# Kernel tuning notes

Measured on AMD Instinct MI355X. Metric: run time of the kernel, lower is better.

The kernel has to match this reference:

```python
import jax, jax.numpy as jnp
from jax import lax
import numpy as np

C_IN, H, W = 9, 11, 11
N_FILT = 64
N_LAYERS = 8
FC_UNITS = 64
LSTM_H = 64
N_ACTIONS = 6
B, T = 32, 128


def setup_inputs() -> dict:
    key = jax.random.key(0)
    ks = jax.random.split(key, 24)
    s = 0.05
    d = {}
    d['x'] = jax.random.normal(ks[0], (B, T, C_IN, H, W), dtype=jnp.float32)
    d['conv0_w'] = jax.random.normal(ks[1], (N_FILT, C_IN, 3, 3), dtype=jnp.float32) * s
    d['conv0_b'] = jnp.zeros((N_FILT,), jnp.float32)
    d['conv_ws'] = jax.random.normal(ks[2], (N_LAYERS - 1, N_FILT, N_FILT, 3, 3), dtype=jnp.float32) * s
    d['conv_bs'] = jnp.zeros((N_LAYERS - 1, N_FILT), jnp.float32)
    d['fc_w'] = jax.random.normal(ks[3], (FC_UNITS, N_FILT * H * W), dtype=jnp.float32) * s
    d['fc_b'] = jnp.zeros((FC_UNITS,), jnp.float32)
    d['w_ih'] = jax.random.normal(ks[4], (4 * LSTM_H, FC_UNITS), dtype=jnp.float32) * s
    d['w_hh'] = jax.random.normal(ks[5], (4 * LSTM_H, LSTM_H), dtype=jnp.float32) * s
    d['b_ih'] = jnp.zeros((4 * LSTM_H,), jnp.float32)
    d['b_hh'] = jnp.zeros((4 * LSTM_H,), jnp.float32)
    d['p1_w'] = jax.random.normal(ks[6], (128, LSTM_H), dtype=jnp.float32) * s
    d['p1_b'] = jnp.zeros((128,), jnp.float32)
    d['p2_w'] = jax.random.normal(ks[7], (N_ACTIONS, 128), dtype=jnp.float32) * s
    d['p2_b'] = jnp.zeros((N_ACTIONS,), jnp.float32)
    d['v1_w'] = jax.random.normal(ks[8], (128, LSTM_H), dtype=jnp.float32) * s
    d['v1_b'] = jnp.zeros((128,), jnp.float32)
    d['v2_w'] = jax.random.normal(ks[9], (1, 128), dtype=jnp.float32) * s
    d['v2_b'] = jnp.zeros((1,), jnp.float32)
    return d


def _conv_relu(h, w, b):
    # h: [N, C, H, W], w: [O, I, 3, 3] -> SAME padding, stride 1
    y = lax.conv_general_dilated(h, w, (1, 1), [(1, 1), (1, 1)],
                                 dimension_numbers=('NCHW', 'OIHW', 'NCHW'))
    return jax.nn.relu(y + b[None, :, None, None])


def _forward(x, conv0_w, conv0_b, conv_ws, conv_bs, fc_w, fc_b,
             w_ih, w_hh, b_ih, b_hh, p1_w, p1_b, p2_w, p2_b, v1_w, v1_b, v2_w, v2_b):
    b, t = x.shape[0], x.shape[1]
    h = x.reshape(b * t, C_IN, H, W)          # batch CNN over all frames at once
    h = _conv_relu(h, conv0_w, conv0_b)
    for i in range(N_LAYERS - 1):             # fixed small layer loop
        h = _conv_relu(h, conv_ws[i], conv_bs[i])
    h = h.reshape(b * t, N_FILT * H * W)
    feats = jax.nn.relu(h @ fc_w.T + fc_b)    # [B*T, FC_UNITS]
    feats = feats.reshape(b, t, FC_UNITS)

    # LSTM (PyTorch gate order i, f, g, o)
    def step(carry, xt):
        hprev, cprev = carry
        g = xt @ w_ih.T + hprev @ w_hh.T + b_ih + b_hh
        i_g, f_g, g_g, o_g = jnp.split(g, 4, axis=-1)
        c = jax.nn.sigmoid(f_g) * cprev + jax.nn.sigmoid(i_g) * jnp.tanh(g_g)
        hn = jax.nn.sigmoid(o_g) * jnp.tanh(c)
        return (hn, c), hn

    h0 = jnp.zeros((b, LSTM_H), feats.dtype)
    c0 = jnp.zeros((b, LSTM_H), feats.dtype)
    _, outs = lax.scan(step, (h0, c0), jnp.swapaxes(feats, 0, 1))  # [T, B, H]
    lstm_out = jnp.swapaxes(outs, 0, 1)       # [B, T, H]

    p = jax.nn.relu(lstm_out @ p1_w.T + p1_b) @ p2_w.T + p2_b  # [B, T, n_actions]
    v = jax.nn.relu(lstm_out @ v1_w.T + v1_b) @ v2_w.T + v2_b  # [B, T, 1]
    return p, v


def reference(x, conv0_w, conv0_b, conv_ws, conv_bs, fc_w, fc_b,
              w_ih, w_hh, b_ih, b_hh, p1_w, p1_b, p2_w, p2_b, v1_w, v1_b, v2_w, v2_b):
    return _forward(x, conv0_w, conv0_b, conv_ws, conv_bs, fc_w, fc_b,
                    w_ih, w_hh, b_ih, b_hh, p1_w, p1_b, p2_w, p2_b,
                    v1_w, v1_b, v2_w, v2_b)
```

## Files before the change

kernel.cpp:

```cpp
#include <hip/hip_runtime.h>
#include <hip/hip_bf16.h>

typedef __attribute__((ext_vector_type(8))) short short8;
typedef __attribute__((ext_vector_type(4))) short short4_t;
typedef __attribute__((ext_vector_type(4))) float floatx4;
typedef __attribute__((ext_vector_type(16))) float floatx16;

#define MFMA_B16(a,b,c) __builtin_amdgcn_mfma_f32_16x16x32_bf16((a),(b),(c),0,0,0)
#define MFMA32(a,b,c)   __builtin_amdgcn_mfma_f32_32x32x16_bf16((a),(b),(c),0,0,0)

__device__ __forceinline__ short f2bf(float f) {
    union { __hip_bfloat16 h; short s; } u;
    u.h = __float2bfloat16(f);
    return u.s;
}

union S8U { short4_t h[2]; short8 v; };

#define N_FRAMES 4096
#define C_IN     9
#define POS      121
#define NF       64
#define FC_K     7744
#define ISTR     20
#define FSZ      10816

#define OFF_W0    0
#define OFF_WP    18432
#define OFF_FCP   534528
#define OFF_WIHT  1525760
#define OFF_BSUM  1591296
#define OFF_ACTS  1592320
#define OFF_XG    66079744
#define OFF_HOUT  70274048

__global__ __launch_bounds__(256) void prep_kernel(
    const float* __restrict__ conv0_w, const float* __restrict__ conv_ws,
    const float* __restrict__ w_ih,
    const float* __restrict__ b_ih, const float* __restrict__ b_hh,
    const float* __restrict__ fc_w,
    short* __restrict__ w0, short* __restrict__ wpk,
    float* __restrict__ wihT, float* __restrict__ bsum,
    short* __restrict__ fcp)
{
    __shared__ float row[FC_K];
    const int tid = threadIdx.x;
    if (blockIdx.x < 64) {
        const int u = blockIdx.x;
        const float* src = fc_w + (size_t)u*FC_K;
        for (int i = tid; i < FC_K; i += 256) row[i] = src[i];
        __syncthreads();
        short* dst = fcp + (size_t)u*FC_K;
        for (int k2 = tid; k2 < FC_K; k2 += 256) {
            int p = k2 >> 6, c = k2 & 63;
            dst[k2] = f2bf(row[c*121 + p]);
        }
        return;
    }
    int idx = (blockIdx.x - 64)*256 + tid;
    if (idx < 9216) {
        int tap = idx >> 10; int r = idx & 1023;
        int mt = r >> 9; int o = (r >> 4) & 31; int ci = r & 15;
        int oc = mt*32 + o;
        float v = (ci < 9) ? conv0_w[(oc*9 + ci)*9 + tap] : 0.f;
        w0[idx] = f2bf(v);
        return;
    }
    idx -= 9216;
    if (idx < 258048) {
        int l = idx / 36864; int r = idx % 36864;
        int tap = r >> 12; int rr = r & 4095;
        int mt = rr >> 11;
        int ks = (rr >> 9) & 3;
        int o  = (rr >> 4) & 31;
        int ci16 = rr & 15;
        int oc = mt*32 + o;
        int ci = ks*16 + ci16;
        wpk[idx] = f2bf(conv_ws[((l*64 + oc)*64 + ci)*9 + tap]);
        return;
    }
    idx -= 258048;
    if (idx < 16384) {
        int k = idx >> 8; int g = idx & 255;
        wihT[idx] = w_ih[g*64 + k];
        return;
    }
    idx -= 16384;
    if (idx < 256) bsum[idx] = b_ih[idx] + b_hh[idx];
}

__global__ __launch_bounds__(128, 3) void conv_stack(
    const float* __restrict__ x,
    const float* __restrict__ conv0_b,
    const float* __restrict__ conv_bs,
    const short* __restrict__ w0,
    const short* __restrict__ wpk,
    short* __restrict__ acts_out)
{
    __shared__ alignas(16) short act[FSZ];
    const int tid  = threadIdx.x;
    const int lane = tid & 63;
    const int wv   = tid >> 6;
    const int n    = lane & 31;
    const int kh   = lane >> 5;
    char* actb = (char*)act;

    const short8 zero8 = {0,0,0,0,0,0,0,0};
    const floatx16 fz16 = {};

    for (int i = tid*8; i < 3392; i += 1024) *(short8*)(&act[i]) = zero8;
    __syncthreads();

    {
        const float* xf = x + (size_t)blockIdx.x*(C_IN*POS);
        for (int i = tid; i < C_IN*POS; i += 128) {
            int ci = i / POS;
            int p  = i - ci*POS;
            int yy = p / 11;
            int xx = p - yy*11;
            act[((yy+1)*13 + (xx+1))*ISTR + ci] = f2bf(xf[i]);
        }
    }
    __syncthreads();

    floatx16 acc[2][2];
    #pragma unroll
    for (int mt=0;mt<2;mt++)
        #pragma unroll
        for (int j=0;j<2;j++) acc[mt][j] = fz16;

    int cell20[2], vbase[2], wbase[2];
    #pragma unroll
    for (int j = 0; j < 2; ++j) {
        int p = (wv*2 + j)*32 + n;
        int pc = (p <= 120) ? p : 120;
        int yy = pc / 11, xx = pc - yy*11;
        int cell = yy*13 + xx;
        cell20[j] = cell*ISTR;
        vbase[j]  = cell*128;
        wbase[j]  = (cell + 14)*128;
    }
    const bool tail = (wv == 1) && (n > 24);

    {
        const short* w0l = w0 + n*16 + kh*8;
        #pragma unroll 1
        for (int dy = 0; dy < 3; ++dy) {
            #pragma unroll 1
            for (int dx = 0; dx < 3; ++dx) {
                const short* wt = w0l + (dy*3+dx)*1024;
                short8 a0 = *(const short8*)(wt);
                short8 a1 = *(const short8*)(wt + 512);
                const int so = (dy*13+dx)*ISTR + kh*8;
                #pragma unroll
                for (int j=0;j<2;j++) {
                    const short* bp = act + cell20[j] + so;
                    S8U t;
                    t.h[0] = *(const short4_t*)(bp);
                    t.h[1] = *(const short4_t*)(bp + 4);
                    acc[0][j] = MFMA32(a0, t.v, acc[0][j]);
                    acc[1][j] = MFMA32(a1, t.v, acc[1][j]);
                }
            }
        }
    }

    __syncthreads();
    for (int i = tid*8; i < FSZ; i += 1024) *(short8*)(&act[i]) = zero8;

    auto epilogue = [&](const float* bias) {
        __syncthreads();
        #pragma unroll
        for (int mt=0;mt<2;mt++) {
            #pragma unroll
            for (int q=0;q<4;q++) {
                const int ch0 = mt*32 + q*8 + kh*4;
                const floatx4 bb = *(const floatx4*)(bias + ch0);
                const int soff = (((mt*4 + q + n) & 7) << 4) + kh*8;
                #pragma unroll
                for (int j=0;j<2;j++) {
                    if (j == 1 && tail) continue;
                    short4_t sv;
                    sv.x = f2bf(fmaxf(acc[mt][j][q*4+0] + bb.x, 0.f));
                    sv.y = f2bf(fmaxf(acc[mt][j][q*4+1] + bb.y, 0.f));
                    sv.z = f2bf(fmaxf(acc[mt][j][q*4+2] + bb.z, 0.f));
                    sv.w = f2bf(fmaxf(acc[mt][j][q*4+3] + bb.w, 0.f));
                    *(short4_t*)(actb + wbase[j] + soff) = sv;
                }
            }
        }
        #pragma unroll
        for (int mt=0;mt<2;mt++)
            #pragma unroll
            for (int j=0;j<2;j++) acc[mt][j] = fz16;
        __syncthreads();
    };

    epilogue(conv0_b);

    {
        short8 AX0,AX1,AX2,AX3, AY0,AY1,AY2,AY3;
        #pragma unroll 1
        for (int l = 1; l < 8; ++l) {
            const short* wl = wpk + (l-1)*36864 + n*16 + kh*8;
            AX0 = *(const short8*)(wl);
            AX1 = *(const short8*)(wl + 2048);
            AX2 = *(const short8*)(wl + 512);
            AX3 = *(const short8*)(wl + 2560);
            #pragma unroll
            for (int i = 0; i < 18; ++i) {
                const int tp = i >> 1, kp = i & 1;
                const int sb_ = ((tp/3)*13 + (tp%3))*128;
                const int cu_ = (tp/3)*11 + (tp%3) + 4 + kh + n + 4*kp;
                const int so0 = sb_ + ((cu_ & 7) << 4);
                const int so1 = sb_ + (((cu_ + 2) & 7) << 4);
                short8 b00 = *(const short8*)(actb + vbase[0] + so0);
                short8 b01 = *(const short8*)(actb + vbase[1] + so0);
                short8 b10 = *(const short8*)(actb + vbase[0] + so1);
                short8 b11 = *(const short8*)(actb + vbase[1] + so1);
                if (i < 17) {
                    const int j = i + 1;
                    const short* wt_ = wl + (j>>1)*4096 + (j&1)*1024;
                    if ((i & 1) == 0) {
                        AY0 = *(const short8*)(wt_);
                        AY1 = *(const short8*)(wt_ + 2048);
                        AY2 = *(const short8*)(wt_ + 512);
                        AY3 = *(const short8*)(wt_ + 2560);
                    } else {
                        AX0 = *(const short8*)(wt_);
                        AX1 = *(const short8*)(wt_ + 2048);
                        AX2 = *(const short8*)(wt_ + 512);
                        AX3 = *(const short8*)(wt_ + 2560);
                    }
                }
                __builtin_amdgcn_sched_barrier(0);
                if ((i & 1) == 0) {
                    acc[0][0]=MFMA32(AX0,b00,acc[0][0]); acc[1][0]=MFMA32(AX1,b00,acc[1][0]);
                    acc[0][1]=MFMA32(AX0,b01,acc[0][1]); acc[1][1]=MFMA32(AX1,b01,acc[1][1]);
                    acc[0][0]=MFMA32(AX2,b10,acc[0][0]); acc[1][0]=MFMA32(AX3,b10,acc[1][0]);
                    acc[0][1]=MFMA32(AX2,b11,acc[0][1]); acc[1][1]=MFMA32(AX3,b11,acc[1][1]);
                } else {
                    acc[0][0]=MFMA32(AY0,b00,acc[0][0]); acc[1][0]=MFMA32(AY1,b00,acc[1][0]);
                    acc[0][1]=MFMA32(AY0,b01,acc[0][1]); acc[1][1]=MFMA32(AY1,b01,acc[1][1]);
                    acc[0][0]=MFMA32(AY2,b10,acc[0][0]); acc[1][0]=MFMA32(AY3,b10,acc[1][0]);
                    acc[0][1]=MFMA32(AY2,b11,acc[0][1]); acc[1][1]=MFMA32(AY3,b11,acc[1][1]);
                }
            }
            epilogue(conv_bs + (l-1)*NF);
        }
    }

    {
        short* dst = acts_out + (size_t)blockIdx.x*FC_K;
        #pragma unroll 1
        for (int it = 0; it < 8; ++it) {
            int q = it*128 + tid;
            if (q < 968) {
                int p = q >> 3, G = q & 7;
                int yy = p / 11, xx = p - yy*11;
                int cell = (yy+1)*13 + (xx+1);
                int slot = (G + p) & 7;
                short8 v = *(const short8*)(actb + cell*128 + slot*16);
                *(short8*)(dst + q*8) = v;
            }
        }
    }
}

__global__ __launch_bounds__(256) void fc_xg_kernel(
    const short* __restrict__ acts, const short* __restrict__ fcp,
    const float* __restrict__ fc_b, const float* __restrict__ wihT,
    const float* __restrict__ bsum, float* __restrict__ xg)
{
    __shared__ alignas(16) float red[3*64*16];
    __shared__ alignas(16) float fbuf[16*64];
    const int tid  = threadIdx.x;
    const int lane = tid & 63;
    const int w    = tid >> 6;
    const int m    = lane & 15;
    const int kg   = lane >> 4;
    const int bm   = blockIdx.x;

    const floatx4 fzero = {0.f,0.f,0.f,0.f};
    floatx4 acc[4];
    #pragma unroll
    for (int nt=0;nt<4;nt++) acc[nt] = fzero;

    const short* arow = acts + (size_t)(bm*16 + m)*FC_K + kg*8;
    const short* brow = fcp + (size_t)m*FC_K + kg*8;

    for (int kc = w; kc < 242; kc += 4) {
        short8 a = *(const short8*)(arow + kc*32);
        #pragma unroll
        for (int nt=0;nt<4;nt++) {
            short8 b = *(const short8*)(brow + (size_t)nt*16*FC_K + kc*32);
            acc[nt] = MFMA_B16(a, b, acc[nt]);
        }
    }

    if (w > 0) {
        #pragma unroll
        for (int nt=0;nt<4;nt++)
            *(floatx4*)(&red[((w-1)*64 + lane)*16 + nt*4]) = acc[nt];
    }
    __syncthreads();
    if (w == 0) {
        #pragma unroll
        for (int nt=0;nt<4;nt++)
            for (int j=0;j<3;j++)
                acc[nt] += *(const floatx4*)(&red[(j*64 + lane)*16 + nt*4]);
        #pragma unroll
        for (int nt=0;nt<4;nt++) {
            int unit = nt*16 + m;
            float bias = fc_b[unit];
            int fr = kg*4;
            fbuf[(fr+0)*NF + unit] = fmaxf(acc[nt].x + bias, 0.f);
            fbuf[(fr+1)*NF + unit] = fmaxf(acc[nt].y + bias, 0.f);
            fbuf[(fr+2)*NF + unit] = fmaxf(acc[nt].z + bias, 0.f);
            fbuf[(fr+3)*NF + unit] = fmaxf(acc[nt].w + bias, 0.f);
        }
    }
    __syncthreads();

    {
        const int g = tid;
        float a[16];
        float bs = bsum[g];
        #pragma unroll
        for (int i=0;i<16;i++) a[i] = bs;
        for (int k=0;k<64;k++) {
            float wk = wihT[k*256 + g];
            #pragma unroll
            for (int i=0;i<16;i++) a[i] += fbuf[i*64 + k] * wk;
        }
        float* xo = xg + (size_t)(bm*16)*256 + g;
        #pragma unroll
        for (int i=0;i<16;i++) xo[i*256] = a[i];
    }
}

__device__ __forceinline__ float sigmf_(float v){
    return __builtin_amdgcn_rcpf(1.f + __expf(-v));
}
__device__ __forceinline__ float tanhf_(float v){
    return 1.f - 2.f*__builtin_amdgcn_rcpf(__expf(2.f*v) + 1.f);
}

__global__ __launch_bounds__(256) void lstm_kernel(
    const float* __restrict__ xg, const float* __restrict__ whh,
    float* __restrict__ hout)
{
    __shared__ alignas(16) float hbuf[64];
    __shared__ alignas(16) float gbuf[256];
    const int g = threadIdx.x;
    const int b = blockIdx.x;

    float4 wv[16];
    #pragma unroll
    for (int k=0;k<16;k++) wv[k] = *(const float4*)(whh + g*64 + k*4);

    float c = 0.f;
    if (g < 64) hbuf[g] = 0.f;
    __syncthreads();

    const float* xr = xg + (size_t)(b*128)*256;
    float nx = xr[g];

    for (int ts=0; ts<128; ++ts) {
        float a0 = nx, a1 = 0.f, a2 = 0.f, a3 = 0.f;
        if (ts + 1 < 128) nx = xr[(ts+1)*256 + g];
        #pragma unroll
        for (int k=0;k<4;k++) {
            float4 h0 = *(const float4*)(&hbuf[k*16]);
            float4 h1 = *(const float4*)(&hbuf[k*16+4]);
            float4 h2 = *(const float4*)(&hbuf[k*16+8]);
            float4 h3 = *(const float4*)(&hbuf[k*16+12]);
            float4 w0 = wv[k*4+0], w1 = wv[k*4+1], w2 = wv[k*4+2], w3 = wv[k*4+3];
            a0 += h0.x*w0.x + h0.y*w0.y + h0.z*w0.z + h0.w*w0.w;
            a1 += h1.x*w1.x + h1.y*w1.y + h1.z*w1.z + h1.w*w1.w;
            a2 += h2.x*w2.x + h2.y*w2.y + h2.z*w2.z + h2.w*w2.w;
            a3 += h3.x*w3.x + h3.y*w3.y + h3.z*w3.z + h3.w*w3.w;
        }
        gbuf[g] = (a0 + a1) + (a2 + a3);
        __syncthreads();
        if (g < 64) {
            float ig = sigmf_(gbuf[g]);
            float fg = sigmf_(gbuf[64+g]);
            float gg = tanhf_(gbuf[128+g]);
            float og = sigmf_(gbuf[192+g]);
            c = fg*c + ig*gg;
            float h = og*tanhf_(c);
            hbuf[g] = h;
            hout[(b*128+ts)*64 + g] = h;
        }
        __syncthreads();
    }
}

__global__ __launch_bounds__(64) void heads_kernel(
    const float* __restrict__ hout,
    const float* __restrict__ p1w, const float* __restrict__ p1b,
    const float* __restrict__ p2w, const float* __restrict__ p2b,
    const float* __restrict__ v1w, const float* __restrict__ v1b,
    const float* __restrict__ v2w, const float* __restrict__ v2b,
    float* __restrict__ out)
{
    __shared__ alignas(16) float hbv[64];
    __shared__ alignas(16) float a1[128];
    __shared__ alignas(16) float a2[128];
    const int lane = threadIdx.x;
    const int f = blockIdx.x;
    hbv[lane] = hout[f*64 + lane];
    __syncthreads();
    #pragma unroll
    for (int uu=0; uu<2; ++uu) {
        const int u = lane + uu*64;
        const float4* wp1 = (const float4*)(p1w + u*64);
        const float4* wv1 = (const float4*)(v1w + u*64);
        float s1a=0.f,s1b=0.f,s1c=0.f,s1d=0.f;
        float s2a=0.f,s2b=0.f,s2c=0.f,s2d=0.f;
        #pragma unroll
        for (int k=0;k<4;k++) {
            float4 h0 = *(const float4*)(&hbv[k*16]);
            float4 h1 = *(const float4*)(&hbv[k*16+4]);
            float4 h2 = *(const float4*)(&hbv[k*16+8]);
            float4 h3 = *(const float4*)(&hbv[k*16+12]);
            float4 w0 = wp1[k*4+0], w1 = wp1[k*4+1], w2 = wp1[k*4+2], w3 = wp1[k*4+3];
            s1a += h0.x*w0.x + h0.y*w0.y + h0.z*w0.z + h0.w*w0.w;
            s1b += h1.x*w1.x + h1.y*w1.y + h1.z*w1.z + h1.w*w1.w;
            s1c += h2.x*w2.x + h2.y*w2.y + h2.z*w2.z + h2.w*w2.w;
            s1d += h3.x*w3.x + h3.y*w3.y + h3.z*w3.z + h3.w*w3.w;
            float4 q0 = wv1[k*4+0], q1 = wv1[k*4+1], q2 = wv1[k*4+2], q3 = wv1[k*4+3];
            s2a += h0.x*q0.x + h0.y*q0.y + h0.z*q0.z + h0.w*q0.w;
            s2b += h1.x*q1.x + h1.y*q1.y + h1.z*q1.z + h1.w*q1.w;
            s2c += h2.x*q2.x + h2.y*q2.y + h2.z*q2.z + h2.w*q2.w;
            s2d += h3.x*q3.x + h3.y*q3.y + h3.z*q3.z + h3.w*q3.w;
        }
        a1[u] = fmaxf(p1b[u] + (s1a+s1b)+(s1c+s1d), 0.f);
        a2[u] = fmaxf(v1b[u] + (s2a+s2b)+(s2c+s2d), 0.f);
    }
    __syncthreads();
    if (lane < 56) {
        const int o = lane >> 3, part = lane & 7;
        const float* src = (o < 6) ? a1 : a2;
        const float* wr  = (o < 6) ? (p2w + o*128) : v2w;
        float s = 0.f;
        const int j0 = part*16;
        #pragma unroll
        for (int j=0;j<16;j++) s += src[j0+j]*wr[j0+j];
        s += __shfl_xor(s, 1);
        s += __shfl_xor(s, 2);
        s += __shfl_xor(s, 4);
        if (part == 0) {
            if (o < 6) out[f*6 + o] = p2b[o] + s;
            else       out[24576 + f] = v2b[0] + s;
        }
    }
}

extern "C" void kernel_launch(void* const* d_in, const int* in_sizes, int n_in,
                              void* d_out, int out_size, void* d_ws, size_t ws_size,
                              hipStream_t stream) {
    const float* x       = (const float*)d_in[0];
    const float* conv0_w = (const float*)d_in[1];
    const float* conv0_b = (const float*)d_in[2];
    const float* conv_ws = (const float*)d_in[3];
    const float* conv_bs = (const float*)d_in[4];
    const float* fc_w    = (const float*)d_in[5];
    const float* fc_b    = (const float*)d_in[6];
    const float* w_ih    = (const float*)d_in[7];
    const float* w_hh    = (const float*)d_in[8];
    const float* b_ih    = (const float*)d_in[9];
    const float* b_hh    = (const float*)d_in[10];
    const float* p1_w    = (const float*)d_in[11];
    const float* p1_b    = (const float*)d_in[12];
    const float* p2_w    = (const float*)d_in[13];
    const float* p2_b    = (const float*)d_in[14];
    const float* v1_w    = (const float*)d_in[15];
    const float* v1_b    = (const float*)d_in[16];
    const float* v2_w    = (const float*)d_in[17];
    const float* v2_b    = (const float*)d_in[18];
    float* out = (float*)d_out;

    char* ws = (char*)d_ws;
    short* w0    = (short*)(ws + OFF_W0);
    short* wpk   = (short*)(ws + OFF_WP);
    short* fcp   = (short*)(ws + OFF_FCP);
    float* wihT  = (float*)(ws + OFF_WIHT);
    float* bsum  = (float*)(ws + OFF_BSUM);
    short* acts  = (short*)(ws + OFF_ACTS);
    float* xgb   = (float*)(ws + OFF_XG);
    float* hout  = (float*)(ws + OFF_HOUT);

    prep_kernel<<<1173, 256, 0, stream>>>(conv0_w, conv_ws, w_ih, b_ih, b_hh,
                                          fc_w, w0, wpk, wihT, bsum, fcp);
    conv_stack<<<N_FRAMES, 128, 0, stream>>>(x, conv0_b, conv_bs, w0, wpk, acts);
    fc_xg_kernel<<<256, 256, 0, stream>>>(acts, fcp, fc_b, wihT, bsum, xgb);
    lstm_kernel<<<32, 256, 0, stream>>>(xgb, w_hh, hout);
    heads_kernel<<<4096, 64, 0, stream>>>(hout, p1_w, p1_b, p2_w, p2_b,
                                          v1_w, v1_b, v2_w, v2_b, out);
}
```

Measured before the change: 500.8 us.

## Double the FC kernel's K-split waves and double-buffer its global loads

The FC+input-gate kernel now launches 512 threads (8 waves) instead of 256, so the 242 K-chunks are split across more waves and the cross-wave reduction buffer grows to match. The MFMA loop is software-pipelined with register double-buffering: loads for the next chunk are issued before the current MFMAs, with sched barriers keeping that order. The w_ih projection epilogue is split across the two halves of the block, and each thread reads fbuf as float4. The aim is to hide global-load latency in a small-grid, memory-bound kernel, at the cost of more registers and a larger LDS reduction.

```diff
diff --git a/kernel.cpp b/kernel.cpp
--- a/kernel.cpp
+++ b/kernel.cpp
@@ -267,12 +267,12 @@
     }
 }
 
-__global__ __launch_bounds__(256) void fc_xg_kernel(
+__global__ __launch_bounds__(512) void fc_xg_kernel(
     const short* __restrict__ acts, const short* __restrict__ fcp,
     const float* __restrict__ fc_b, const float* __restrict__ wihT,
     const float* __restrict__ bsum, float* __restrict__ xg)
 {
-    __shared__ alignas(16) float red[3*64*16];
+    __shared__ alignas(16) float red[7*64*16];
     __shared__ alignas(16) float fbuf[16*64];
     const int tid  = threadIdx.x;
     const int lane = tid & 63;
@@ -289,12 +289,46 @@
     const short* arow = acts + (size_t)(bm*16 + m)*FC_K + kg*8;
     const short* brow = fcp + (size_t)m*FC_K + kg*8;
 
-    for (int kc = w; kc < 242; kc += 4) {
-        short8 a = *(const short8*)(arow + kc*32);
-        #pragma unroll
-        for (int nt=0;nt<4;nt++) {
-            short8 b = *(const short8*)(brow + (size_t)nt*16*FC_K + kc*32);
-            acc[nt] = MFMA_B16(a, b, acc[nt]);
+    {
+        short8 aX, aY, bX0,bX1,bX2,bX3, bY0,bY1,bY2,bY3;
+        int kc = w;
+        if (kc < 242) {
+            aX  = *(const short8*)(arow + (size_t)kc*32);
+            bX0 = *(const short8*)(brow + (size_t)kc*32);
+            bX1 = *(const short8*)(brow + (size_t)16*FC_K + (size_t)kc*32);
+            bX2 = *(const short8*)(brow + (size_t)32*FC_K + (size_t)kc*32);
+            bX3 = *(const short8*)(brow + (size_t)48*FC_K + (size_t)kc*32);
+        }
+        while (kc < 242) {
+            int k2 = kc + 8;
+            if (k2 < 242) {
+                aY  = *(const short8*)(arow + (size_t)k2*32);
+                bY0 = *(const short8*)(brow + (size_t)k2*32);
+                bY1 = *(const short8*)(brow + (size_t)16*FC_K + (size_t)k2*32);
+                bY2 = *(const short8*)(brow + (size_t)32*FC_K + (size_t)k2*32);
+                bY3 = *(const short8*)(brow + (size_t)48*FC_K + (size_t)k2*32);
+            }
+            __builtin_amdgcn_sched_barrier(0);
+            acc[0] = MFMA_B16(aX, bX0, acc[0]);
+            acc[1] = MFMA_B16(aX, bX1, acc[1]);
+            acc[2] = MFMA_B16(aX, bX2, acc[2]);
+            acc[3] = MFMA_B16(aX, bX3, acc[3]);
+            kc = k2;
+            if (kc >= 242) break;
+            int k3 = kc + 8;
+            if (k3 < 242) {
+                aX  = *(const short8*)(arow + (size_t)k3*32);
+                bX0 = *(const short8*)(brow + (size_t)k3*32);
+                bX1 = *(const short8*)(brow + (size_t)16*FC_K + (size_t)k3*32);
+                bX2 = *(const short8*)(brow + (size_t)32*FC_K + (size_t)k3*32);
+                bX3 = *(const short8*)(brow + (size_t)48*FC_K + (size_t)k3*32);
+            }
+            __builtin_amdgcn_sched_barrier(0);
+            acc[0] = MFMA_B16(aY, bY0, acc[0]);
+            acc[1] = MFMA_B16(aY, bY1, acc[1]);
+            acc[2] = MFMA_B16(aY, bY2, acc[2]);
+            acc[3] = MFMA_B16(aY, bY3, acc[3]);
+            kc = k3;
         }
     }
 
@@ -307,7 +341,7 @@
     if (w == 0) {
         #pragma unroll
         for (int nt=0;nt<4;nt++)
-            for (int j=0;j<3;j++)
+            for (int j=0;j<7;j++)
                 acc[nt] += *(const floatx4*)(&red[(j*64 + lane)*16 + nt*4]);
         #pragma unroll
         for (int nt=0;nt<4;nt++) {
@@ -323,19 +357,27 @@
     __syncthreads();
 
     {
-        const int g = tid;
-        float a[16];
+        const int g = tid & 255;
+        const int half = tid >> 8;
+        const int fb = half*8;
+        float a[8];
         float bs = bsum[g];
         #pragma unroll
-        for (int i=0;i<16;i++) a[i] = bs;
-        for (int k=0;k<64;k++) {
-            float wk = wihT[k*256 + g];
+        for (int j=0;j<8;j++) a[j] = bs;
+        for (int k4=0;k4<16;k4++) {
+            float wk0 = wihT[(k4*4+0)*256 + g];
+            float wk1 = wihT[(k4*4+1)*256 + g];
+            float wk2 = wihT[(k4*4+2)*256 + g];
+            float wk3 = wihT[(k4*4+3)*256 + g];
             #pragma unroll
-            for (int i=0;i<16;i++) a[i] += fbuf[i*64 + k] * wk;
-        }
-        float* xo = xg + (size_t)(bm*16)*256 + g;
-        #pragma unroll
-        for (int i=0;i<16;i++) xo[i*256] = a[i];
+            for (int j=0;j<8;j++) {
+                float4 f = *(const float4*)(&fbuf[(fb+j)*64 + k4*4]);
+                a[j] += f.x*wk0 + f.y*wk1 + f.z*wk2 + f.w*wk3;
+            }
+        }
+        float* xo = xg + (size_t)(bm*16 + fb)*256 + g;
+        #pragma unroll
+        for (int j=0;j<8;j++) xo[j*256] = a[j];
     }
 }
 
@@ -495,7 +537,7 @@
     prep_kernel<<<1173, 256, 0, stream>>>(conv0_w, conv_ws, w_ih, b_ih, b_hh,
                                           fc_w, w0, wpk, wihT, bsum, fcp);
     conv_stack<<<N_FRAMES, 128, 0, stream>>>(x, conv0_b, conv_bs, w0, wpk, acts);
-    fc_xg_kernel<<<256, 256, 0, stream>>>(acts, fcp, fc_b, wihT, bsum, xgb);
+    fc_xg_kernel<<<256, 512, 0, stream>>>(acts, fcp, fc_b, wihT, bsum, xgb);
     lstm_kernel<<<32, 256, 0, stream>>>(xgb, w_hh, hout);
     heads_kernel<<<4096, 64, 0, stream>>>(hout, p1_w, p1_b, p2_w, p2_b,
                                           v1_w, v1_b, v2_w, v2_b, out);
```

Result: no change. 496.3 us (-0.9%).
